# Kernel optimization log

Measured on AMD Instinct MI355X. Metric: run time of the kernel, lower is better.

Reference implementation:

```python
import jax, jax.numpy as jnp
import numpy as np

N_EMBD = 1024
N_HEAD = 16
LN_EPS = 1e-5

def setup_inputs() -> dict:
    key = jax.random.key(0)
    ks = jax.random.split(key, 12)
    B, T, C = 2, 2048, N_EMBD
    s = lambda k, shape, scale=0.02: (jax.random.normal(k, shape, dtype=jnp.float32) * scale)
    return {
        "x": jax.random.normal(ks[0], (B, T, C), dtype=jnp.float32),
        "ln1_g": jnp.ones((C,), jnp.float32),
        "ln1_b": jnp.zeros((C,), jnp.float32),
        "W_attn": s(ks[1], (C, 3 * C)),
        "b_attn": jnp.zeros((3 * C,), jnp.float32),
        "W_o": s(ks[2], (C, C)),
        "b_o": jnp.zeros((C,), jnp.float32),
        "ln2_g": jnp.ones((C,), jnp.float32),
        "ln2_b": jnp.zeros((C,), jnp.float32),
        "W_fc": s(ks[3], (C, 4 * C)),
        "b_fc": jnp.zeros((4 * C,), jnp.float32),
        "W_fc2": s(ks[4], (4 * C, C)),
        "b_fc2": jnp.zeros((C,), jnp.float32),
    }

def _layernorm(x, g, b):
    mu = jnp.mean(x, axis=-1, keepdims=True)
    var = jnp.mean(jnp.square(x - mu), axis=-1, keepdims=True)
    return (x - mu) * jax.lax.rsqrt(var + LN_EPS) * g + b

def reference(x, ln1_g, ln1_b, W_attn, b_attn, W_o, b_o, ln2_g, ln2_b, W_fc, b_fc, W_fc2, b_fc2):
    B, T, C = x.shape
    H, D = N_HEAD, C // N_HEAD
    # ---- attention branch (use_cache=False: T_total == T, causal mask) ----
    h = _layernorm(x, ln1_g, ln1_b)
    qkv = h @ W_attn + b_attn                       # [B,T,3C]
    q, k, v = jnp.split(qkv, 3, axis=-1)
    q = q.reshape(B, T, H, D).transpose(0, 2, 1, 3)  # [B,H,T,D]
    k = k.reshape(B, T, H, D).transpose(0, 2, 1, 3)
    v = v.reshape(B, T, H, D).transpose(0, 2, 1, 3)
    w = jnp.einsum('bhqd,bhkd->bhqk', q, k) / jnp.sqrt(jnp.float32(D))  # [B,H,T,T]
    causal = jnp.tril(jnp.ones((T, T), dtype=bool))
    w = jnp.where(causal, w, jnp.float32(-jnp.inf))
    w = jax.nn.softmax(w, axis=-1)
    y = jnp.einsum('bhqk,bhkd->bhqd', w, v)          # [B,H,T,D]
    y = y.transpose(0, 2, 1, 3).reshape(B, T, C)
    x = x + (y @ W_o + b_o)
    # ---- MLP branch ----
    h2 = _layernorm(x, ln2_g, ln2_b)
    h2 = jax.nn.gelu(h2 @ W_fc + b_fc, approximate=True)  # tanh approx, matches nn.GELU('tanh')
    x = x + (h2 @ W_fc2 + b_fc2)
    return x
```

## Files before the change

### kernel.cpp

```cpp
#include <hip/hip_runtime.h>


typedef unsigned short u16;
typedef unsigned int u32;
typedef __attribute__((ext_vector_type(8))) short v8s;
typedef __attribute__((ext_vector_type(4))) float v4f;

#define GAS __attribute__((address_space(1)))
#define LAS __attribute__((address_space(3)))

__device__ __forceinline__ u16 f2bf(float f) {
  u32 u = __float_as_uint(f);
  u = (u + 0x7FFF + ((u >> 16) & 1)) >> 16;
  return (u16)u;
}
__device__ __forceinline__ float bf2f(u16 h) {
  return __uint_as_float(((u32)h) << 16);
}
__device__ __forceinline__ float fast_tanh(float x) {
  return 1.f - 2.f / (1.f + __expf(2.f * x));
}

__global__ __launch_bounds__(256)
void wtrans(const float* __restrict__ W, u16* __restrict__ Wt, int K, int N) {
  __shared__ float tile[32][33];
  const int n0 = blockIdx.x << 5, k0 = blockIdx.y << 5;
  const int r = threadIdx.x >> 5, c = threadIdx.x & 31;
#pragma unroll
  for (int i = 0; i < 4; ++i)
    tile[r + 8 * i][c] = W[(size_t)(k0 + r + 8 * i) * N + n0 + c];
  __syncthreads();
#pragma unroll
  for (int i = 0; i < 4; ++i)
    Wt[(size_t)(n0 + r + 8 * i) * K + k0 + c] = f2bf(tile[c][r + 8 * i]);
}

__global__ __launch_bounds__(256)
void ln_bf16(const float* __restrict__ x, const float* __restrict__ g,
             const float* __restrict__ be, u16* __restrict__ out) {
  constexpr int C = 1024;
  const int row = blockIdx.x, t = threadIdx.x;
  const float4 v = ((const float4*)(x + (size_t)row * C))[t];
  float s = v.x + v.y + v.z + v.w;
#pragma unroll
  for (int m = 32; m >= 1; m >>= 1) s += __shfl_xor(s, m);
  __shared__ float red[4], red2[4];
  if ((t & 63) == 0) red[t >> 6] = s;
  __syncthreads();
  const float mu = (red[0] + red[1] + red[2] + red[3]) * (1.f / C);
  const float dx = v.x - mu, dy = v.y - mu, dz = v.z - mu, dw = v.w - mu;
  float s2 = dx * dx + dy * dy + dz * dz + dw * dw;
#pragma unroll
  for (int m = 32; m >= 1; m >>= 1) s2 += __shfl_xor(s2, m);
  if ((t & 63) == 0) red2[t >> 6] = s2;
  __syncthreads();
  const float var = (red2[0] + red2[1] + red2[2] + red2[3]) * (1.f / C);
  const float rs = rsqrtf(var + 1e-5f);
  const int c = t << 2;
  u16 o0 = f2bf(dx * rs * g[c + 0] + be[c + 0]);
  u16 o1 = f2bf(dy * rs * g[c + 1] + be[c + 1]);
  u16 o2 = f2bf(dz * rs * g[c + 2] + be[c + 2]);
  u16 o3 = f2bf(dw * rs * g[c + 3] + be[c + 3]);
  uint2 pk;
  pk.x = (u32)o0 | ((u32)o1 << 16);
  pk.y = (u32)o2 | ((u32)o3 << 16);
  *(uint2*)(out + (size_t)row * C + c) = pk;
}

template <int EPI>
__global__ __launch_bounds__(256)
void gemm_bt_p(const u16* __restrict__ A, const u16* __restrict__ Bt,
               const float* __restrict__ bias, const float* __restrict__ res,
               void* __restrict__ outp, int M, int N, int K) {
  __shared__ u16 As[4][128 * 32];
  __shared__ u16 Bs[4][128 * 32];
  const int tid = threadIdx.x;
  const int wave = tid >> 6, lane = tid & 63;
  const int m0 = blockIdx.y << 7, n0 = blockIdx.x << 7;

  v4f acc[4][4];
  const v4f vz = {0.f, 0.f, 0.f, 0.f};
#pragma unroll
  for (int i = 0; i < 4; ++i)
#pragma unroll
    for (int j = 0; j < 4; ++j) acc[i][j] = vz;

  const int wm = (wave >> 1) << 6, wn = (wave & 1) << 6;
  const int sr = lane >> 2;
  const int sc = (lane & 3) << 3;
  const int fr = lane & 15;
  const int fk = (lane >> 4) << 3;
  const int c0 = wave << 1;

  const u16* gA0 = A + (size_t)(m0 + c0 * 16 + sr) * K + sc;
  const u16* gA1 = A + (size_t)(m0 + c0 * 16 + 16 + sr) * K + sc;
  const u16* gB0 = Bt + (size_t)(n0 + c0 * 16 + sr) * K + sc;
  const u16* gB1 = Bt + (size_t)(n0 + c0 * 16 + 16 + sr) * K + sc;
  const int aoff = c0 * 512;

  const u32 asb = (u32)(size_t)(LAS const u16*)&As[0][0];
  const u32 bsb = (u32)(size_t)(LAS const u16*)&Bs[0][0];
  const u32 afrag = (u32)(((wm + fr) << 6) + (fk << 1));
  const u32 bfrag = (u32)(((wn + fr) << 6) + (fk << 1));

  const int nk = K >> 5;

#define P128_ISSUE(t, bf)                                                        \
  do {                                                                           \
    const int k0_ = (t) << 5;                                                    \
    __builtin_amdgcn_global_load_lds((GAS const u32*)(gA0 + k0_),                \
                                     (LAS u32*)(As[bf] + aoff), 16, 0, 0);       \
    __builtin_amdgcn_global_load_lds((GAS const u32*)(gA1 + k0_),                \
                                     (LAS u32*)(As[bf] + aoff + 512), 16, 0, 0); \
    __builtin_amdgcn_global_load_lds((GAS const u32*)(gB0 + k0_),                \
                                     (LAS u32*)(Bs[bf] + aoff), 16, 0, 0);       \
    __builtin_amdgcn_global_load_lds((GAS const u32*)(gB1 + k0_),                \
                                     (LAS u32*)(Bs[bf] + aoff + 512), 16, 0, 0); \
  } while (0)

  P128_ISSUE(0, 0);
  P128_ISSUE(1, 1);
  P128_ISSUE(2, 2);

  auto compute = [&](int kt) __attribute__((always_inline)) {
    const u32 ab = asb + ((u32)(kt & 3) << 13) + afrag;
    const u32 bb = bsb + ((u32)(kt & 3) << 13) + bfrag;
    v8s a0, a1, a2, a3, b0, b1, b2, b3;
    asm volatile("ds_read_b128 %0, %1 offset:0"    : "=v"(a0) : "v"(ab));
    asm volatile("ds_read_b128 %0, %1 offset:1024" : "=v"(a1) : "v"(ab));
    asm volatile("ds_read_b128 %0, %1 offset:2048" : "=v"(a2) : "v"(ab));
    asm volatile("ds_read_b128 %0, %1 offset:3072" : "=v"(a3) : "v"(ab));
    asm volatile("ds_read_b128 %0, %1 offset:0"    : "=v"(b0) : "v"(bb));
    asm volatile("ds_read_b128 %0, %1 offset:1024" : "=v"(b1) : "v"(bb));
    asm volatile("ds_read_b128 %0, %1 offset:2048" : "=v"(b2) : "v"(bb));
    asm volatile("ds_read_b128 %0, %1 offset:3072" : "=v"(b3) : "v"(bb));
    asm volatile("s_waitcnt lgkmcnt(0)"
                 : "+v"(a0), "+v"(a1), "+v"(a2), "+v"(a3),
                   "+v"(b0), "+v"(b1), "+v"(b2), "+v"(b3)
                 :
                 : "memory");
    acc[0][0] = __builtin_amdgcn_mfma_f32_16x16x32_bf16(a0, b0, acc[0][0], 0, 0, 0);
    acc[0][1] = __builtin_amdgcn_mfma_f32_16x16x32_bf16(a0, b1, acc[0][1], 0, 0, 0);
    acc[0][2] = __builtin_amdgcn_mfma_f32_16x16x32_bf16(a0, b2, acc[0][2], 0, 0, 0);
    acc[0][3] = __builtin_amdgcn_mfma_f32_16x16x32_bf16(a0, b3, acc[0][3], 0, 0, 0);
    acc[1][0] = __builtin_amdgcn_mfma_f32_16x16x32_bf16(a1, b0, acc[1][0], 0, 0, 0);
    acc[1][1] = __builtin_amdgcn_mfma_f32_16x16x32_bf16(a1, b1, acc[1][1], 0, 0, 0);
    acc[1][2] = __builtin_amdgcn_mfma_f32_16x16x32_bf16(a1, b2, acc[1][2], 0, 0, 0);
    acc[1][3] = __builtin_amdgcn_mfma_f32_16x16x32_bf16(a1, b3, acc[1][3], 0, 0, 0);
    acc[2][0] = __builtin_amdgcn_mfma_f32_16x16x32_bf16(a2, b0, acc[2][0], 0, 0, 0);
    acc[2][1] = __builtin_amdgcn_mfma_f32_16x16x32_bf16(a2, b1, acc[2][1], 0, 0, 0);
    acc[2][2] = __builtin_amdgcn_mfma_f32_16x16x32_bf16(a2, b2, acc[2][2], 0, 0, 0);
    acc[2][3] = __builtin_amdgcn_mfma_f32_16x16x32_bf16(a2, b3, acc[2][3], 0, 0, 0);
    acc[3][0] = __builtin_amdgcn_mfma_f32_16x16x32_bf16(a3, b0, acc[3][0], 0, 0, 0);
    acc[3][1] = __builtin_amdgcn_mfma_f32_16x16x32_bf16(a3, b1, acc[3][1], 0, 0, 0);
    acc[3][2] = __builtin_amdgcn_mfma_f32_16x16x32_bf16(a3, b2, acc[3][2], 0, 0, 0);
    acc[3][3] = __builtin_amdgcn_mfma_f32_16x16x32_bf16(a3, b3, acc[3][3], 0, 0, 0);
  };

  for (int kt = 0; kt < nk - 3; ++kt) {
    asm volatile("s_waitcnt vmcnt(8)" ::: "memory");
    __builtin_amdgcn_s_barrier();
    P128_ISSUE(kt + 3, (kt + 3) & 3);
    compute(kt);
  }
  asm volatile("s_waitcnt vmcnt(8)" ::: "memory");
  __builtin_amdgcn_s_barrier();
  compute(nk - 3);
  asm volatile("s_waitcnt vmcnt(4)" ::: "memory");
  __builtin_amdgcn_s_barrier();
  compute(nk - 2);
  asm volatile("s_waitcnt vmcnt(0)" ::: "memory");
  __builtin_amdgcn_s_barrier();
  compute(nk - 1);
#undef P128_ISSUE

  const int er = (lane >> 4) << 2;
#pragma unroll
  for (int mi = 0; mi < 4; ++mi) {
#pragma unroll
    for (int ni = 0; ni < 4; ++ni) {
      const int col = n0 + wn + ni * 16 + fr;
      const float bcol = bias[col];
#pragma unroll
      for (int r = 0; r < 4; ++r) {
        const int row = m0 + wm + mi * 16 + er + r;
        float v = acc[mi][ni][r] + bcol;
        if constexpr (EPI == 1) {
          const float t = fast_tanh(0.7978845608028654f * (v + 0.044715f * v * v * v));
          v = 0.5f * v * (1.f + t);
        }
        if constexpr (EPI == 2) {
          v += res[(size_t)row * N + col];
          ((float*)outp)[(size_t)row * N + col] = v;
        } else {
          ((u16*)outp)[(size_t)row * N + col] = f2bf(v);
        }
      }
    }
  }
}

template <int EPI>
__global__ __launch_bounds__(256)
void gemm_bt_p6(const u16* __restrict__ A, const u16* __restrict__ Bt,
                const float* __restrict__ bias, const float* __restrict__ res,
                void* __restrict__ outp, int M, int N, int K) {
  __shared__ u16 As[6][128 * 32];
  __shared__ u16 Bs[6][128 * 32];
  const int tid = threadIdx.x;
  const int wave = tid >> 6, lane = tid & 63;
  const int wg = blockIdx.y * (int)gridDim.x + blockIdx.x;
  const int xcd = wg & 7;
  const int seq = wg >> 3;
  const int bx = seq & 7;
  const int by = ((seq >> 3) << 3) + xcd;
  const int m0 = by << 7, n0 = bx << 7;

  v4f acc[4][4];
  const v4f vz = {0.f, 0.f, 0.f, 0.f};
#pragma unroll
  for (int i = 0; i < 4; ++i)
#pragma unroll
    for (int j = 0; j < 4; ++j) acc[i][j] = vz;

  const int wm = (wave >> 1) << 6, wn = (wave & 1) << 6;
  const int sr = lane >> 2;
  const int sc = (lane & 3) << 3;
  const int fr = lane & 15;
  const int fk = (lane >> 4) << 3;
  const int c0 = wave << 1;

  const u16* gA0 = A + (size_t)(m0 + c0 * 16 + sr) * K + sc;
  const u16* gA1 = A + (size_t)(m0 + c0 * 16 + 16 + sr) * K + sc;
  const u16* gB0 = Bt + (size_t)(n0 + c0 * 16 + sr) * K + sc;
  const u16* gB1 = Bt + (size_t)(n0 + c0 * 16 + 16 + sr) * K + sc;
  const int aoff = c0 * 512;

  const u32 asb = (u32)(size_t)(LAS const u16*)&As[0][0];
  const u32 bsb = (u32)(size_t)(LAS const u16*)&Bs[0][0];
  const u32 afrag = (u32)(((wm + fr) << 6) + (fk << 1));
  const u32 bfrag = (u32)(((wn + fr) << 6) + (fk << 1));

  const int nk = K >> 5;

#define P6_ISSUE(t, bf)                                                          \
  do {                                                                           \
    const int k0_ = (t) << 5;                                                    \
    __builtin_amdgcn_global_load_lds((GAS const u32*)(gA0 + k0_),                \
                                     (LAS u32*)(As[bf] + aoff), 16, 0, 0);       \
    __builtin_amdgcn_global_load_lds((GAS const u32*)(gA1 + k0_),                \
                                     (LAS u32*)(As[bf] + aoff + 512), 16, 0, 0); \
    __builtin_amdgcn_global_load_lds((GAS const u32*)(gB0 + k0_),                \
                                     (LAS u32*)(Bs[bf] + aoff), 16, 0, 0);       \
    __builtin_amdgcn_global_load_lds((GAS const u32*)(gB1 + k0_),                \
                                     (LAS u32*)(Bs[bf] + aoff + 512), 16, 0, 0); \
  } while (0)

  P6_ISSUE(0, 0);
  P6_ISSUE(1, 1);
  P6_ISSUE(2, 2);
  P6_ISSUE(3, 3);
  P6_ISSUE(4, 4);

  auto compute = [&](int cbuf) __attribute__((always_inline)) {
    const u32 ab = asb + ((u32)cbuf << 13) + afrag;
    const u32 bb = bsb + ((u32)cbuf << 13) + bfrag;
    v8s a0, a1, a2, a3, b0, b1, b2, b3;
    asm volatile("ds_read_b128 %0, %1 offset:0"    : "=v"(a0) : "v"(ab));
    asm volatile("ds_read_b128 %0, %1 offset:1024" : "=v"(a1) : "v"(ab));
    asm volatile("ds_read_b128 %0, %1 offset:2048" : "=v"(a2) : "v"(ab));
    asm volatile("ds_read_b128 %0, %1 offset:3072" : "=v"(a3) : "v"(ab));
    asm volatile("ds_read_b128 %0, %1 offset:0"    : "=v"(b0) : "v"(bb));
    asm volatile("ds_read_b128 %0, %1 offset:1024" : "=v"(b1) : "v"(bb));
    asm volatile("ds_read_b128 %0, %1 offset:2048" : "=v"(b2) : "v"(bb));
    asm volatile("ds_read_b128 %0, %1 offset:3072" : "=v"(b3) : "v"(bb));
    asm volatile("s_waitcnt lgkmcnt(0)"
                 : "+v"(a0), "+v"(a1), "+v"(a2), "+v"(a3),
                   "+v"(b0), "+v"(b1), "+v"(b2), "+v"(b3)
                 :
                 : "memory");
    acc[0][0] = __builtin_amdgcn_mfma_f32_16x16x32_bf16(a0, b0, acc[0][0], 0, 0, 0);
    acc[0][1] = __builtin_amdgcn_mfma_f32_16x16x32_bf16(a0, b1, acc[0][1], 0, 0, 0);
    acc[0][2] = __builtin_amdgcn_mfma_f32_16x16x32_bf16(a0, b2, acc[0][2], 0, 0, 0);
    acc[0][3] = __builtin_amdgcn_mfma_f32_16x16x32_bf16(a0, b3, acc[0][3], 0, 0, 0);
    acc[1][0] = __builtin_amdgcn_mfma_f32_16x16x32_bf16(a1, b0, acc[1][0], 0, 0, 0);
    acc[1][1] = __builtin_amdgcn_mfma_f32_16x16x32_bf16(a1, b1, acc[1][1], 0, 0, 0);
    acc[1][2] = __builtin_amdgcn_mfma_f32_16x16x32_bf16(a1, b2, acc[1][2], 0, 0, 0);
    acc[1][3] = __builtin_amdgcn_mfma_f32_16x16x32_bf16(a1, b3, acc[1][3], 0, 0, 0);
    acc[2][0] = __builtin_amdgcn_mfma_f32_16x16x32_bf16(a2, b0, acc[2][0], 0, 0, 0);
    acc[2][1] = __builtin_amdgcn_mfma_f32_16x16x32_bf16(a2, b1, acc[2][1], 0, 0, 0);
    acc[2][2] = __builtin_amdgcn_mfma_f32_16x16x32_bf16(a2, b2, acc[2][2], 0, 0, 0);
    acc[2][3] = __builtin_amdgcn_mfma_f32_16x16x32_bf16(a2, b3, acc[2][3], 0, 0, 0);
    acc[3][0] = __builtin_amdgcn_mfma_f32_16x16x32_bf16(a3, b0, acc[3][0], 0, 0, 0);
    acc[3][1] = __builtin_amdgcn_mfma_f32_16x16x32_bf16(a3, b1, acc[3][1], 0, 0, 0);
    acc[3][2] = __builtin_amdgcn_mfma_f32_16x16x32_bf16(a3, b2, acc[3][2], 0, 0, 0);
    acc[3][3] = __builtin_amdgcn_mfma_f32_16x16x32_bf16(a3, b3, acc[3][3], 0, 0, 0);
  };

  int cb = 0;
  int pb = 5;
  for (int kt = 0; kt < nk - 5; ++kt) {
    asm volatile("s_waitcnt vmcnt(16)" ::: "memory");
    __builtin_amdgcn_s_barrier();
    P6_ISSUE(kt + 5, pb);
    compute(cb);
    cb = (cb == 5) ? 0 : cb + 1;
    pb = (pb == 5) ? 0 : pb + 1;
  }
  asm volatile("s_waitcnt vmcnt(16)" ::: "memory");
  __builtin_amdgcn_s_barrier();
  compute(cb); cb = (cb == 5) ? 0 : cb + 1;
  asm volatile("s_waitcnt vmcnt(12)" ::: "memory");
  __builtin_amdgcn_s_barrier();
  compute(cb); cb = (cb == 5) ? 0 : cb + 1;
  asm volatile("s_waitcnt vmcnt(8)" ::: "memory");
  __builtin_amdgcn_s_barrier();
  compute(cb); cb = (cb == 5) ? 0 : cb + 1;
  asm volatile("s_waitcnt vmcnt(4)" ::: "memory");
  __builtin_amdgcn_s_barrier();
  compute(cb); cb = (cb == 5) ? 0 : cb + 1;
  asm volatile("s_waitcnt vmcnt(0)" ::: "memory");
  __builtin_amdgcn_s_barrier();
  compute(cb);
#undef P6_ISSUE

  const int er = (lane >> 4) << 2;
#pragma unroll
  for (int mi = 0; mi < 4; ++mi) {
#pragma unroll
    for (int ni = 0; ni < 4; ++ni) {
      const int col = n0 + wn + ni * 16 + fr;
      const float bcol = bias[col];
#pragma unroll
      for (int r = 0; r < 4; ++r) {
        const int row = m0 + wm + mi * 16 + er + r;
        float v = acc[mi][ni][r] + bcol;
        if constexpr (EPI == 1) {
          const float t = fast_tanh(0.7978845608028654f * (v + 0.044715f * v * v * v));
          v = 0.5f * v * (1.f + t);
        }
        if constexpr (EPI == 2) {
          v += res[(size_t)row * N + col];
          ((float*)outp)[(size_t)row * N + col] = v;
        } else {
          ((u16*)outp)[(size_t)row * N + col] = f2bf(v);
        }
      }
    }
  }
}

template <int EPI>
__global__ __launch_bounds__(256)
void gemm_bt_n64(const u16* __restrict__ A, const u16* __restrict__ Bt,
                 const float* __restrict__ bias, const float* __restrict__ res,
                 void* __restrict__ outp, int M, int N, int K) {
  __shared__ u16 As[4][128 * 32];
  __shared__ u16 Bs[4][64 * 32];
  const int tid = threadIdx.x;
  const int wave = tid >> 6, lane = tid & 63;
  const int m0 = blockIdx.y << 7, n0 = blockIdx.x << 6;

  v4f acc[4][2];
  const v4f vz = {0.f, 0.f, 0.f, 0.f};
#pragma unroll
  for (int i = 0; i < 4; ++i)
#pragma unroll
    for (int j = 0; j < 2; ++j) acc[i][j] = vz;

  const int wm = (wave >> 1) << 6, wn = (wave & 1) << 5;
  const int sr = lane >> 2;
  const int sc = (lane & 3) << 3;
  const int fr = lane & 15;
  const int fk = (lane >> 4) << 3;

  const u16* gA0 = A + (size_t)(m0 + wave * 32 + sr) * K + sc;
  const u16* gA1 = A + (size_t)(m0 + wave * 32 + 16 + sr) * K + sc;
  const u16* gB0 = Bt + (size_t)(n0 + wave * 16 + sr) * K + sc;
  const int aoff = wave * 1024;
  const int boff = wave * 512;

  const u32 asb = (u32)(size_t)(LAS const u16*)&As[0][0];
  const u32 bsb = (u32)(size_t)(LAS const u16*)&Bs[0][0];
  const u32 afrag = (u32)(((wm + fr) << 6) + (fk << 1));
  const u32 bfrag = (u32)(((wn + fr) << 6) + (fk << 1));

  const int nk = K >> 5;

#define N64_ISSUE(t, bf)                                                      \
  do {                                                                        \
    const int k0_ = (t) << 5;                                                 \
    __builtin_amdgcn_global_load_lds((GAS const u32*)(gA0 + k0_),             \
                                     (LAS u32*)(As[bf] + aoff), 16, 0, 0);    \
    __builtin_amdgcn_global_load_lds((GAS const u32*)(gA1 + k0_),             \
                                     (LAS u32*)(As[bf] + aoff + 512), 16, 0, 0); \
    __builtin_amdgcn_global_load_lds((GAS const u32*)(gB0 + k0_),             \
                                     (LAS u32*)(Bs[bf] + boff), 16, 0, 0);    \
  } while (0)

  N64_ISSUE(0, 0);
  N64_ISSUE(1, 1);
  N64_ISSUE(2, 2);

  auto compute = [&](int kt) __attribute__((always_inline)) {
    const u32 ab = asb + ((u32)(kt & 3) << 13) + afrag;
    const u32 bb = bsb + ((u32)(kt & 3) << 12) + bfrag;
    v8s a0, a1, a2, a3, b0, b1;
    asm volatile("ds_read_b128 %0, %1 offset:0"    : "=v"(a0) : "v"(ab));
    asm volatile("ds_read_b128 %0, %1 offset:1024" : "=v"(a1) : "v"(ab));
    asm volatile("ds_read_b128 %0, %1 offset:2048" : "=v"(a2) : "v"(ab));
    asm volatile("ds_read_b128 %0, %1 offset:3072" : "=v"(a3) : "v"(ab));
    asm volatile("ds_read_b128 %0, %1 offset:0"    : "=v"(b0) : "v"(bb));
    asm volatile("ds_read_b128 %0, %1 offset:1024" : "=v"(b1) : "v"(bb));
    asm volatile("s_waitcnt lgkmcnt(0)"
                 : "+v"(a0), "+v"(a1), "+v"(a2), "+v"(a3), "+v"(b0), "+v"(b1)
                 :
                 : "memory");
    acc[0][0] = __builtin_amdgcn_mfma_f32_16x16x32_bf16(a0, b0, acc[0][0], 0, 0, 0);
    acc[0][1] = __builtin_amdgcn_mfma_f32_16x16x32_bf16(a0, b1, acc[0][1], 0, 0, 0);
    acc[1][0] = __builtin_amdgcn_mfma_f32_16x16x32_bf16(a1, b0, acc[1][0], 0, 0, 0);
    acc[1][1] = __builtin_amdgcn_mfma_f32_16x16x32_bf16(a1, b1, acc[1][1], 0, 0, 0);
    acc[2][0] = __builtin_amdgcn_mfma_f32_16x16x32_bf16(a2, b0, acc[2][0], 0, 0, 0);
    acc[2][1] = __builtin_amdgcn_mfma_f32_16x16x32_bf16(a2, b1, acc[2][1], 0, 0, 0);
    acc[3][0] = __builtin_amdgcn_mfma_f32_16x16x32_bf16(a3, b0, acc[3][0], 0, 0, 0);
    acc[3][1] = __builtin_amdgcn_mfma_f32_16x16x32_bf16(a3, b1, acc[3][1], 0, 0, 0);
  };

  for (int kt = 0; kt < nk - 2; ++kt) {
    asm volatile("s_waitcnt vmcnt(6)" ::: "memory");
    __builtin_amdgcn_s_barrier();
    if (kt + 3 < nk) N64_ISSUE(kt + 3, (kt + 3) & 3);
    compute(kt);
  }
  asm volatile("s_waitcnt vmcnt(3)" ::: "memory");
  __builtin_amdgcn_s_barrier();
  compute(nk - 2);
  asm volatile("s_waitcnt vmcnt(0)" ::: "memory");
  __builtin_amdgcn_s_barrier();
  compute(nk - 1);
#undef N64_ISSUE

  const int er = (lane >> 4) << 2;
#pragma unroll
  for (int mi = 0; mi < 4; ++mi) {
#pragma unroll
    for (int ni = 0; ni < 2; ++ni) {
      const int col = n0 + wn + ni * 16 + fr;
      const float bcol = bias[col];
#pragma unroll
      for (int r = 0; r < 4; ++r) {
        const int row = m0 + wm + mi * 16 + er + r;
        float v = acc[mi][ni][r] + bcol;
        if constexpr (EPI == 1) {
          const float t = fast_tanh(0.7978845608028654f * (v + 0.044715f * v * v * v));
          v = 0.5f * v * (1.f + t);
        }
        if constexpr (EPI == 2) {
          v += res[(size_t)row * N + col];
          ((float*)outp)[(size_t)row * N + col] = v;
        } else {
          ((u16*)outp)[(size_t)row * N + col] = f2bf(v);
        }
      }
    }
  }
}

__global__ __launch_bounds__(256)
void transpose_v(const u16* __restrict__ qkv, u16* __restrict__ Vt) {
  __shared__ u16 tile[64][65];
  const int t0 = blockIdx.x << 6;
  const int bh = blockIdx.y;
  const int b = bh >> 4, h = bh & 15;
  const int r4 = threadIdx.x >> 6, c = threadIdx.x & 63;
#pragma unroll
  for (int i = 0; i < 16; ++i) {
    const int r = r4 * 16 + i;
    tile[r][c] = qkv[(size_t)(b * 2048 + t0 + r) * 3072 + 2048 + h * 64 + c];
  }
  __syncthreads();
#pragma unroll
  for (int i = 0; i < 16; ++i) {
    const int d = r4 * 16 + i;
    Vt[(size_t)bh * 64 * 2048 + (size_t)d * 2048 + t0 + c] = tile[c][d];
  }
}

constexpr int PSTR = 88;

template <bool MASKED>
__device__ __forceinline__ void attn_sub(
    const v8s (&kf)[4][2], const v8s (&vfr)[4][2], const v8s (&qf)[2],
    v4f (&ot)[4], float& m_i, float& l_i, u16* __restrict__ pw,
    const int kb, const int qrow, const int fr, const int fg) {
  const v4f vz = {0.f, 0.f, 0.f, 0.f};
  v4f st[4];
#pragma unroll
  for (int ks = 0; ks < 4; ++ks) {
    st[ks] = vz;
    st[ks] = __builtin_amdgcn_mfma_f32_16x16x32_bf16(kf[ks][0], qf[0], st[ks], 0, 0, 0);
    st[ks] = __builtin_amdgcn_mfma_f32_16x16x32_bf16(kf[ks][1], qf[1], st[ks], 0, 0, 0);
  }
  const int q = qrow + fr;
  float e[4][4];
  float mt = -1e30f;
#pragma unroll
  for (int ks = 0; ks < 4; ++ks)
#pragma unroll
    for (int r = 0; r < 4; ++r) {
      float v = st[ks][r] * 0.125f;
      if (MASKED) v = (kb + ks * 16 + fg * 4 + r <= q) ? v : -1e30f;
      e[ks][r] = v;
      mt = fmaxf(mt, v);
    }
  mt = fmaxf(mt, __shfl_xor(mt, 16));
  mt = fmaxf(mt, __shfl_xor(mt, 32));
  const float m_new = fmaxf(m_i, mt);
  const float alpha = __expf(m_i - m_new);
  m_i = m_new;
  float ls = 0.f;
#pragma unroll
  for (int ks = 0; ks < 4; ++ks)
#pragma unroll
    for (int r = 0; r < 4; ++r) {
      e[ks][r] = __expf(e[ks][r] - m_new);
      ls += e[ks][r];
    }
  ls += __shfl_xor(ls, 16);
  ls += __shfl_xor(ls, 32);
  l_i = l_i * alpha + ls;
#pragma unroll
  for (int ds = 0; ds < 4; ++ds) ot[ds] *= alpha;
#pragma unroll
  for (int ks = 0; ks < 4; ++ks) {
    ushort4 pk4;
    pk4.x = f2bf(e[ks][0]);
    pk4.y = f2bf(e[ks][1]);
    pk4.z = f2bf(e[ks][2]);
    pk4.w = f2bf(e[ks][3]);
    *(ushort4*)&pw[fr * PSTR + ks * 16 + fg * 4] = pk4;
  }
  const v8s pf0 = *(const v8s*)&pw[fr * PSTR + fg * 8];
  const v8s pf1 = *(const v8s*)&pw[fr * PSTR + 32 + fg * 8];
#pragma unroll
  for (int ds = 0; ds < 4; ++ds) {
    ot[ds] = __builtin_amdgcn_mfma_f32_16x16x32_bf16(vfr[ds][0], pf0, ot[ds], 0, 0, 0);
    ot[ds] = __builtin_amdgcn_mfma_f32_16x16x32_bf16(vfr[ds][1], pf1, ot[ds], 0, 0, 0);
  }
}

__global__ __launch_bounds__(256)
void attn_kernel(const u16* __restrict__ qkv, const u16* __restrict__ Vt,
                 u16* __restrict__ y) {
  constexpr int T = 2048, D = 64, C = 1024, QS = 3072;
  __shared__ alignas(16) u16 Ktile[2][64 * 64];
  __shared__ alignas(16) u16 Vtile[2][64 * 64];
  __shared__ alignas(16) u16 Pw[4][16 * PSTR];

  const int tid = threadIdx.x, wave = tid >> 6, lane = tid & 63;
  const int fr = lane & 15, fg = lane >> 4;
  const int bh = blockIdx.y, b = bh >> 4, h = bh & 15;
  const int ta = blockIdx.x, tb = 31 - ta;
  const u16* qkvb = qkv + (size_t)b * T * QS + h * 64;
  const u16* Kg = qkvb + 1024;
  const u16* Vh = Vt + (size_t)bh * D * T;
  u16* pw = &Pw[wave][0];

  const int rowA = ta * 64 + wave * 16;
  const int rowB = tb * 64 + wave * 16;

  v8s qfA[2], qfB[2];
#pragma unroll
  for (int dh = 0; dh < 2; ++dh) {
    qfA[dh] = *(const v8s*)&qkvb[(size_t)(rowA + fr) * QS + dh * 32 + fg * 8];
    qfB[dh] = *(const v8s*)&qkvb[(size_t)(rowB + fr) * QS + dh * 32 + fg * 8];
  }

  const v4f vz = {0.f, 0.f, 0.f, 0.f};
  v4f otA[4], otB[4];
#pragma unroll
  for (int ds = 0; ds < 4; ++ds) { otA[ds] = vz; otB[ds] = vz; }
  float mA = -1e30f, lA = 0.f, mB = -1e30f, lB = 0.f;

  const int srow = lane >> 3;
  const int sg0 = lane & 7;

  const int nt = tb + 1;
  {
#pragma unroll
    for (int cc = 0; cc < 2; ++cc) {
      const int r0 = wave * 16 + cc * 8;
      const int rr = r0 + srow;
      const int gg = sg0 ^ (rr & 7);
      __builtin_amdgcn_global_load_lds(
          (GAS const u32*)(Kg + (size_t)rr * QS + gg * 8),
          (LAS u32*)(Ktile[0] + r0 * 64), 16, 0, 0);
      __builtin_amdgcn_global_load_lds(
          (GAS const u32*)(Vh + (size_t)rr * T + gg * 8),
          (LAS u32*)(Vtile[0] + r0 * 64), 16, 0, 0);
    }
  }
  for (int kt = 0; kt < nt; ++kt) {
    __syncthreads();
    if (kt + 1 < nt) {
      const int kb1 = (kt + 1) << 6;
      const int nb = (kt + 1) & 1;
#pragma unroll
      for (int cc = 0; cc < 2; ++cc) {
        const int r0 = wave * 16 + cc * 8;
        const int rr = r0 + srow;
        const int gg = sg0 ^ (rr & 7);
        __builtin_amdgcn_global_load_lds(
            (GAS const u32*)(Kg + (size_t)(kb1 + rr) * QS + gg * 8),
            (LAS u32*)(Ktile[nb] + r0 * 64), 16, 0, 0);
        __builtin_amdgcn_global_load_lds(
            (GAS const u32*)(Vh + (size_t)rr * T + kb1 + gg * 8),
            (LAS u32*)(Vtile[nb] + r0 * 64), 16, 0, 0);
      }
    }
    const u16* Kt = Ktile[kt & 1];
    const u16* Vi = Vtile[kt & 1];
    const int kb = kt << 6;
    const int swz = fr & 7;
    v8s kf[4][2], vfr[4][2];
#pragma unroll
    for (int ks = 0; ks < 4; ++ks) {
      const int rr = ks * 16 + fr;
      kf[ks][0] = *(const v8s*)&Kt[rr * 64 + ((0 + fg) ^ swz) * 8];
      kf[ks][1] = *(const v8s*)&Kt[rr * 64 + ((4 + fg) ^ swz) * 8];
      vfr[ks][0] = *(const v8s*)&Vi[rr * 64 + ((0 + fg) ^ swz) * 8];
      vfr[ks][1] = *(const v8s*)&Vi[rr * 64 + ((4 + fg) ^ swz) * 8];
    }
    if (kt < ta) {
      attn_sub<false>(kf, vfr, qfA, otA, mA, lA, pw, kb, rowA, fr, fg);
      attn_sub<false>(kf, vfr, qfB, otB, mB, lB, pw, kb, rowB, fr, fg);
    } else if (kt == ta) {
      attn_sub<true>(kf, vfr, qfA, otA, mA, lA, pw, kb, rowA, fr, fg);
      attn_sub<false>(kf, vfr, qfB, otB, mB, lB, pw, kb, rowB, fr, fg);
    } else if (kt < tb) {
      attn_sub<false>(kf, vfr, qfB, otB, mB, lB, pw, kb, rowB, fr, fg);
    } else {
      attn_sub<true>(kf, vfr, qfB, otB, mB, lB, pw, kb, rowB, fr, fg);
    }
  }

  const float invA = 1.f / lA, invB = 1.f / lB;
#pragma unroll
  for (int ds = 0; ds < 4; ++ds) {
    ushort4 a4, b4;
    a4.x = f2bf(otA[ds][0] * invA);
    a4.y = f2bf(otA[ds][1] * invA);
    a4.z = f2bf(otA[ds][2] * invA);
    a4.w = f2bf(otA[ds][3] * invA);
    b4.x = f2bf(otB[ds][0] * invB);
    b4.y = f2bf(otB[ds][1] * invB);
    b4.z = f2bf(otB[ds][2] * invB);
    b4.w = f2bf(otB[ds][3] * invB);
    *(ushort4*)&y[(size_t)(b * T + rowA + fr) * C + h * D + ds * 16 + fg * 4] = a4;
    *(ushort4*)&y[(size_t)(b * T + rowB + fr) * C + h * D + ds * 16 + fg * 4] = b4;
  }
}

extern "C" void kernel_launch(void* const* d_in, const int* in_sizes, int n_in,
                              void* d_out, int out_size, void* d_ws, size_t ws_size,
                              hipStream_t stream) {
  const float* x      = (const float*)d_in[0];
  const float* ln1_g  = (const float*)d_in[1];
  const float* ln1_b  = (const float*)d_in[2];
  const float* W_attn = (const float*)d_in[3];
  const float* b_attn = (const float*)d_in[4];
  const float* W_o    = (const float*)d_in[5];
  const float* b_o    = (const float*)d_in[6];
  const float* ln2_g  = (const float*)d_in[7];
  const float* ln2_b  = (const float*)d_in[8];
  const float* W_fc   = (const float*)d_in[9];
  const float* b_fc   = (const float*)d_in[10];
  const float* W_fc2  = (const float*)d_in[11];
  const float* b_fc2  = (const float*)d_in[12];
  float* out = (float*)d_out;
  char* ws = (char*)d_ws;

  const size_t MB = 1u << 20;
  u16* Wattn_t = (u16*)(ws + 0 * MB);
  u16* Wo_t    = (u16*)(ws + 6 * MB);
  u16* Wfc_t   = (u16*)(ws + 8 * MB);
  u16* Wfc2_t  = (u16*)(ws + 16 * MB);
  float* x1    = (float*)(ws + 24 * MB);
  u16* h1      = (u16*)(ws + 40 * MB);
  u16* qkv     = (u16*)(ws + 48 * MB);
  u16* Vt      = (u16*)(ws + 88 * MB);
  u16* yb      = (u16*)(ws + 40 * MB);
  u16* h2      = (u16*)(ws + 48 * MB);
  u16* ab      = (u16*)(ws + 56 * MB);

  wtrans<<<dim3(3072 / 32, 1024 / 32), 256, 0, stream>>>(W_attn, Wattn_t, 1024, 3072);
  wtrans<<<dim3(1024 / 32, 1024 / 32), 256, 0, stream>>>(W_o, Wo_t, 1024, 1024);
  wtrans<<<dim3(4096 / 32, 1024 / 32), 256, 0, stream>>>(W_fc, Wfc_t, 1024, 4096);
  wtrans<<<dim3(1024 / 32, 4096 / 32), 256, 0, stream>>>(W_fc2, Wfc2_t, 4096, 1024);

  ln_bf16<<<4096, 256, 0, stream>>>(x, ln1_g, ln1_b, h1);
  gemm_bt_p<0><<<dim3(3072 / 128, 4096 / 128), 256, 0, stream>>>(
      h1, Wattn_t, b_attn, nullptr, qkv, 4096, 3072, 1024);
  transpose_v<<<dim3(2048 / 64, 32), 256, 0, stream>>>(qkv, Vt);
  attn_kernel<<<dim3(16, 32), 256, 0, stream>>>(qkv, Vt, yb);
  gemm_bt_n64<2><<<dim3(1024 / 64, 4096 / 128), 256, 0, stream>>>(
      yb, Wo_t, b_o, x, x1, 4096, 1024, 1024);
  ln_bf16<<<4096, 256, 0, stream>>>(x1, ln2_g, ln2_b, h2);
  gemm_bt_p<1><<<dim3(4096 / 128, 4096 / 128), 256, 0, stream>>>(
      h2, Wfc_t, b_fc, nullptr, ab, 4096, 4096, 1024);
  gemm_bt_p6<2><<<dim3(1024 / 128, 4096 / 128), 256, 0, stream>>>(
      ab, Wfc2_t, b_fc2, x1, out, 4096, 1024, 4096);
}
```

Before: 363.0 us.

## Double-buffer LDS fragments in GEMM and fold p6 kernel into templated gemm_bt_p

The 128x128 GEMM mainloop now reads the next k-step's LDS fragments into a second register set while the MFMAs for the current step run. A sched_barrier keeps the ordering fixed so LDS read latency hides behind matrix math. The separate 6-stage gemm_bt_p6 kernel is removed, and the FC2 GEMM now uses the 4-stage kernel with an XCD-aware block remap template flag. This costs extra VGPRs for the second fragment set, and FC2 loses its deeper global prefetch.

```diff
diff --git a/kernel.cpp b/kernel.cpp
--- a/kernel.cpp
+++ b/kernel.cpp
@@ -67,7 +67,7 @@
   *(uint2*)(out + (size_t)row * C + c) = pk;
 }
 
-template <int EPI>
+template <int EPI, int REMAP>
 __global__ __launch_bounds__(256)
 void gemm_bt_p(const u16* __restrict__ A, const u16* __restrict__ Bt,
                const float* __restrict__ bias, const float* __restrict__ res,
@@ -76,7 +76,18 @@
   __shared__ u16 Bs[4][128 * 32];
   const int tid = threadIdx.x;
   const int wave = tid >> 6, lane = tid & 63;
-  const int m0 = blockIdx.y << 7, n0 = blockIdx.x << 7;
+  int bx, by;
+  if constexpr (REMAP) {
+    const int wg = blockIdx.y * (int)gridDim.x + blockIdx.x;
+    const int xcd = wg & 7;
+    const int seq = wg >> 3;
+    bx = seq & 7;
+    by = ((seq >> 3) << 3) + xcd;
+  } else {
+    bx = blockIdx.x;
+    by = blockIdx.y;
+  }
+  const int m0 = by << 7, n0 = bx << 7;
 
   v4f acc[4][4];
   const v4f vz = {0.f, 0.f, 0.f, 0.f};
@@ -118,211 +129,66 @@
                                      (LAS u32*)(Bs[bf] + aoff + 512), 16, 0, 0); \
   } while (0)
 
+  auto ldfr = [&](int kt, v8s (&a)[4], v8s (&b)[4]) __attribute__((always_inline)) {
+    const u32 ab = asb + ((u32)(kt & 3) << 13) + afrag;
+    const u32 bb = bsb + ((u32)(kt & 3) << 13) + bfrag;
+    asm volatile("ds_read_b128 %0, %1 offset:0"    : "=v"(a[0]) : "v"(ab));
+    asm volatile("ds_read_b128 %0, %1 offset:1024" : "=v"(a[1]) : "v"(ab));
+    asm volatile("ds_read_b128 %0, %1 offset:2048" : "=v"(a[2]) : "v"(ab));
+    asm volatile("ds_read_b128 %0, %1 offset:3072" : "=v"(a[3]) : "v"(ab));
+    asm volatile("ds_read_b128 %0, %1 offset:0"    : "=v"(b[0]) : "v"(bb));
+    asm volatile("ds_read_b128 %0, %1 offset:1024" : "=v"(b[1]) : "v"(bb));
+    asm volatile("ds_read_b128 %0, %1 offset:2048" : "=v"(b[2]) : "v"(bb));
+    asm volatile("ds_read_b128 %0, %1 offset:3072" : "=v"(b[3]) : "v"(bb));
+  };
+  auto wait8 = [&](v8s (&a)[4], v8s (&b)[4]) __attribute__((always_inline)) {
+    asm volatile("s_waitcnt lgkmcnt(0)"
+                 : "+v"(a[0]), "+v"(a[1]), "+v"(a[2]), "+v"(a[3]),
+                   "+v"(b[0]), "+v"(b[1]), "+v"(b[2]), "+v"(b[3])
+                 :
+                 : "memory");
+  };
+  auto mfma16 = [&](v8s (&a)[4], v8s (&b)[4]) __attribute__((always_inline)) {
+#pragma unroll
+    for (int i = 0; i < 4; ++i)
+#pragma unroll
+      for (int j = 0; j < 4; ++j)
+        acc[i][j] = __builtin_amdgcn_mfma_f32_16x16x32_bf16(a[i], b[j], acc[i][j], 0, 0, 0);
+  };
+
+  v8s aX[4], bX[4], aY[4], bY[4];
+
   P128_ISSUE(0, 0);
   P128_ISSUE(1, 1);
   P128_ISSUE(2, 2);
-
-  auto compute = [&](int kt) __attribute__((always_inline)) {
-    const u32 ab = asb + ((u32)(kt & 3) << 13) + afrag;
-    const u32 bb = bsb + ((u32)(kt & 3) << 13) + bfrag;
-    v8s a0, a1, a2, a3, b0, b1, b2, b3;
-    asm volatile("ds_read_b128 %0, %1 offset:0"    : "=v"(a0) : "v"(ab));
-    asm volatile("ds_read_b128 %0, %1 offset:1024" : "=v"(a1) : "v"(ab));
-    asm volatile("ds_read_b128 %0, %1 offset:2048" : "=v"(a2) : "v"(ab));
-    asm volatile("ds_read_b128 %0, %1 offset:3072" : "=v"(a3) : "v"(ab));
-    asm volatile("ds_read_b128 %0, %1 offset:0"    : "=v"(b0) : "v"(bb));
-    asm volatile("ds_read_b128 %0, %1 offset:1024" : "=v"(b1) : "v"(bb));
-    asm volatile("ds_read_b128 %0, %1 offset:2048" : "=v"(b2) : "v"(bb));
-    asm volatile("ds_read_b128 %0, %1 offset:3072" : "=v"(b3) : "v"(bb));
-    asm volatile("s_waitcnt lgkmcnt(0)"
-                 : "+v"(a0), "+v"(a1), "+v"(a2), "+v"(a3),
-                   "+v"(b0), "+v"(b1), "+v"(b2), "+v"(b3)
-                 :
-                 : "memory");
-    acc[0][0] = __builtin_amdgcn_mfma_f32_16x16x32_bf16(a0, b0, acc[0][0], 0, 0, 0);
-    acc[0][1] = __builtin_amdgcn_mfma_f32_16x16x32_bf16(a0, b1, acc[0][1], 0, 0, 0);
-    acc[0][2] = __builtin_amdgcn_mfma_f32_16x16x32_bf16(a0, b2, acc[0][2], 0, 0, 0);
-    acc[0][3] = __builtin_amdgcn_mfma_f32_16x16x32_bf16(a0, b3, acc[0][3], 0, 0, 0);
-    acc[1][0] = __builtin_amdgcn_mfma_f32_16x16x32_bf16(a1, b0, acc[1][0], 0, 0, 0);
-    acc[1][1] = __builtin_amdgcn_mfma_f32_16x16x32_bf16(a1, b1, acc[1][1], 0, 0, 0);
-    acc[1][2] = __builtin_amdgcn_mfma_f32_16x16x32_bf16(a1, b2, acc[1][2], 0, 0, 0);
-    acc[1][3] = __builtin_amdgcn_mfma_f32_16x16x32_bf16(a1, b3, acc[1][3], 0, 0, 0);
-    acc[2][0] = __builtin_amdgcn_mfma_f32_16x16x32_bf16(a2, b0, acc[2][0], 0, 0, 0);
-    acc[2][1] = __builtin_amdgcn_mfma_f32_16x16x32_bf16(a2, b1, acc[2][1], 0, 0, 0);
-    acc[2][2] = __builtin_amdgcn_mfma_f32_16x16x32_bf16(a2, b2, acc[2][2], 0, 0, 0);
-    acc[2][3] = __builtin_amdgcn_mfma_f32_16x16x32_bf16(a2, b3, acc[2][3], 0, 0, 0);
-    acc[3][0] = __builtin_amdgcn_mfma_f32_16x16x32_bf16(a3, b0, acc[3][0], 0, 0, 0);
-    acc[3][1] = __builtin_amdgcn_mfma_f32_16x16x32_bf16(a3, b1, acc[3][1], 0, 0, 0);
-    acc[3][2] = __builtin_amdgcn_mfma_f32_16x16x32_bf16(a3, b2, acc[3][2], 0, 0, 0);
-    acc[3][3] = __builtin_amdgcn_mfma_f32_16x16x32_bf16(a3, b3, acc[3][3], 0, 0, 0);
-  };
-
-  for (int kt = 0; kt < nk - 3; ++kt) {
-    asm volatile("s_waitcnt vmcnt(8)" ::: "memory");
-    __builtin_amdgcn_s_barrier();
-    P128_ISSUE(kt + 3, (kt + 3) & 3);
-    compute(kt);
-  }
   asm volatile("s_waitcnt vmcnt(8)" ::: "memory");
   __builtin_amdgcn_s_barrier();
-  compute(nk - 3);
-  asm volatile("s_waitcnt vmcnt(4)" ::: "memory");
-  __builtin_amdgcn_s_barrier();
-  compute(nk - 2);
+  ldfr(0, aX, bX);
+  wait8(aX, bX);
+
+  auto step4 = [&](int k, v8s (&ca)[4], v8s (&cb)[4],
+                   v8s (&na)[4], v8s (&nb)[4]) __attribute__((always_inline)) {
+    asm volatile("s_waitcnt vmcnt(4)" ::: "memory");
+    __builtin_amdgcn_s_barrier();
+    ldfr(k + 1, na, nb);
+    if (k + 3 < nk) P128_ISSUE(k + 3, (k + 3) & 3);
+    __builtin_amdgcn_sched_barrier(0);
+    mfma16(ca, cb);
+    wait8(na, nb);
+  };
+
+  for (int kt = 0; kt < nk - 2; kt += 2) {
+    step4(kt, aX, bX, aY, bY);
+    step4(kt + 1, aY, bY, aX, bX);
+  }
   asm volatile("s_waitcnt vmcnt(0)" ::: "memory");
   __builtin_amdgcn_s_barrier();
-  compute(nk - 1);
+  ldfr(nk - 1, aY, bY);
+  __builtin_amdgcn_sched_barrier(0);
+  mfma16(aX, bX);
+  wait8(aY, bY);
+  mfma16(aY, bY);
 #undef P128_ISSUE
-
-  const int er = (lane >> 4) << 2;
-#pragma unroll
-  for (int mi = 0; mi < 4; ++mi) {
-#pragma unroll
-    for (int ni = 0; ni < 4; ++ni) {
-      const int col = n0 + wn + ni * 16 + fr;
-      const float bcol = bias[col];
-#pragma unroll
-      for (int r = 0; r < 4; ++r) {
-        const int row = m0 + wm + mi * 16 + er + r;
-        float v = acc[mi][ni][r] + bcol;
-        if constexpr (EPI == 1) {
-          const float t = fast_tanh(0.7978845608028654f * (v + 0.044715f * v * v * v));
-          v = 0.5f * v * (1.f + t);
-        }
-        if constexpr (EPI == 2) {
-          v += res[(size_t)row * N + col];
-          ((float*)outp)[(size_t)row * N + col] = v;
-        } else {
-          ((u16*)outp)[(size_t)row * N + col] = f2bf(v);
-        }
-      }
-    }
-  }
-}
-
-template <int EPI>
-__global__ __launch_bounds__(256)
-void gemm_bt_p6(const u16* __restrict__ A, const u16* __restrict__ Bt,
-                const float* __restrict__ bias, const float* __restrict__ res,
-                void* __restrict__ outp, int M, int N, int K) {
-  __shared__ u16 As[6][128 * 32];
-  __shared__ u16 Bs[6][128 * 32];
-  const int tid = threadIdx.x;
-  const int wave = tid >> 6, lane = tid & 63;
-  const int wg = blockIdx.y * (int)gridDim.x + blockIdx.x;
-  const int xcd = wg & 7;
-  const int seq = wg >> 3;
-  const int bx = seq & 7;
-  const int by = ((seq >> 3) << 3) + xcd;
-  const int m0 = by << 7, n0 = bx << 7;
-
-  v4f acc[4][4];
-  const v4f vz = {0.f, 0.f, 0.f, 0.f};
-#pragma unroll
-  for (int i = 0; i < 4; ++i)
-#pragma unroll
-    for (int j = 0; j < 4; ++j) acc[i][j] = vz;
-
-  const int wm = (wave >> 1) << 6, wn = (wave & 1) << 6;
-  const int sr = lane >> 2;
-  const int sc = (lane & 3) << 3;
-  const int fr = lane & 15;
-  const int fk = (lane >> 4) << 3;
-  const int c0 = wave << 1;
-
-  const u16* gA0 = A + (size_t)(m0 + c0 * 16 + sr) * K + sc;
-  const u16* gA1 = A + (size_t)(m0 + c0 * 16 + 16 + sr) * K + sc;
-  const u16* gB0 = Bt + (size_t)(n0 + c0 * 16 + sr) * K + sc;
-  const u16* gB1 = Bt + (size_t)(n0 + c0 * 16 + 16 + sr) * K + sc;
-  const int aoff = c0 * 512;
-
-  const u32 asb = (u32)(size_t)(LAS const u16*)&As[0][0];
-  const u32 bsb = (u32)(size_t)(LAS const u16*)&Bs[0][0];
-  const u32 afrag = (u32)(((wm + fr) << 6) + (fk << 1));
-  const u32 bfrag = (u32)(((wn + fr) << 6) + (fk << 1));
-
-  const int nk = K >> 5;
-
-#define P6_ISSUE(t, bf)                                                          \
-  do {                                                                           \
-    const int k0_ = (t) << 5;                                                    \
-    __builtin_amdgcn_global_load_lds((GAS const u32*)(gA0 + k0_),                \
-                                     (LAS u32*)(As[bf] + aoff), 16, 0, 0);       \
-    __builtin_amdgcn_global_load_lds((GAS const u32*)(gA1 + k0_),                \
-                                     (LAS u32*)(As[bf] + aoff + 512), 16, 0, 0); \
-    __builtin_amdgcn_global_load_lds((GAS const u32*)(gB0 + k0_),                \
-                                     (LAS u32*)(Bs[bf] + aoff), 16, 0, 0);       \
-    __builtin_amdgcn_global_load_lds((GAS const u32*)(gB1 + k0_),                \
-                                     (LAS u32*)(Bs[bf] + aoff + 512), 16, 0, 0); \
-  } while (0)
-
-  P6_ISSUE(0, 0);
-  P6_ISSUE(1, 1);
-  P6_ISSUE(2, 2);
-  P6_ISSUE(3, 3);
-  P6_ISSUE(4, 4);
-
-  auto compute = [&](int cbuf) __attribute__((always_inline)) {
-    const u32 ab = asb + ((u32)cbuf << 13) + afrag;
-    const u32 bb = bsb + ((u32)cbuf << 13) + bfrag;
-    v8s a0, a1, a2, a3, b0, b1, b2, b3;
-    asm volatile("ds_read_b128 %0, %1 offset:0"    : "=v"(a0) : "v"(ab));
-    asm volatile("ds_read_b128 %0, %1 offset:1024" : "=v"(a1) : "v"(ab));
-    asm volatile("ds_read_b128 %0, %1 offset:2048" : "=v"(a2) : "v"(ab));
-    asm volatile("ds_read_b128 %0, %1 offset:3072" : "=v"(a3) : "v"(ab));
-    asm volatile("ds_read_b128 %0, %1 offset:0"    : "=v"(b0) : "v"(bb));
-    asm volatile("ds_read_b128 %0, %1 offset:1024" : "=v"(b1) : "v"(bb));
-    asm volatile("ds_read_b128 %0, %1 offset:2048" : "=v"(b2) : "v"(bb));
-    asm volatile("ds_read_b128 %0, %1 offset:3072" : "=v"(b3) : "v"(bb));
-    asm volatile("s_waitcnt lgkmcnt(0)"
-                 : "+v"(a0), "+v"(a1), "+v"(a2), "+v"(a3),
-                   "+v"(b0), "+v"(b1), "+v"(b2), "+v"(b3)
-                 :
-                 : "memory");
-    acc[0][0] = __builtin_amdgcn_mfma_f32_16x16x32_bf16(a0, b0, acc[0][0], 0, 0, 0);
-    acc[0][1] = __builtin_amdgcn_mfma_f32_16x16x32_bf16(a0, b1, acc[0][1], 0, 0, 0);
-    acc[0][2] = __builtin_amdgcn_mfma_f32_16x16x32_bf16(a0, b2, acc[0][2], 0, 0, 0);
-    acc[0][3] = __builtin_amdgcn_mfma_f32_16x16x32_bf16(a0, b3, acc[0][3], 0, 0, 0);
-    acc[1][0] = __builtin_amdgcn_mfma_f32_16x16x32_bf16(a1, b0, acc[1][0], 0, 0, 0);
-    acc[1][1] = __builtin_amdgcn_mfma_f32_16x16x32_bf16(a1, b1, acc[1][1], 0, 0, 0);
-    acc[1][2] = __builtin_amdgcn_mfma_f32_16x16x32_bf16(a1, b2, acc[1][2], 0, 0, 0);
-    acc[1][3] = __builtin_amdgcn_mfma_f32_16x16x32_bf16(a1, b3, acc[1][3], 0, 0, 0);
-    acc[2][0] = __builtin_amdgcn_mfma_f32_16x16x32_bf16(a2, b0, acc[2][0], 0, 0, 0);
-    acc[2][1] = __builtin_amdgcn_mfma_f32_16x16x32_bf16(a2, b1, acc[2][1], 0, 0, 0);
-    acc[2][2] = __builtin_amdgcn_mfma_f32_16x16x32_bf16(a2, b2, acc[2][2], 0, 0, 0);
-    acc[2][3] = __builtin_amdgcn_mfma_f32_16x16x32_bf16(a2, b3, acc[2][3], 0, 0, 0);
-    acc[3][0] = __builtin_amdgcn_mfma_f32_16x16x32_bf16(a3, b0, acc[3][0], 0, 0, 0);
-    acc[3][1] = __builtin_amdgcn_mfma_f32_16x16x32_bf16(a3, b1, acc[3][1], 0, 0, 0);
-    acc[3][2] = __builtin_amdgcn_mfma_f32_16x16x32_bf16(a3, b2, acc[3][2], 0, 0, 0);
-    acc[3][3] = __builtin_amdgcn_mfma_f32_16x16x32_bf16(a3, b3, acc[3][3], 0, 0, 0);
-  };
-
-  int cb = 0;
-  int pb = 5;
-  for (int kt = 0; kt < nk - 5; ++kt) {
-    asm volatile("s_waitcnt vmcnt(16)" ::: "memory");
-    __builtin_amdgcn_s_barrier();
-    P6_ISSUE(kt + 5, pb);
-    compute(cb);
-    cb = (cb == 5) ? 0 : cb + 1;
-    pb = (pb == 5) ? 0 : pb + 1;
-  }
-  asm volatile("s_waitcnt vmcnt(16)" ::: "memory");
-  __builtin_amdgcn_s_barrier();
-  compute(cb); cb = (cb == 5) ? 0 : cb + 1;
-  asm volatile("s_waitcnt vmcnt(12)" ::: "memory");
-  __builtin_amdgcn_s_barrier();
-  compute(cb); cb = (cb == 5) ? 0 : cb + 1;
-  asm volatile("s_waitcnt vmcnt(8)" ::: "memory");
-  __builtin_amdgcn_s_barrier();
-  compute(cb); cb = (cb == 5) ? 0 : cb + 1;
-  asm volatile("s_waitcnt vmcnt(4)" ::: "memory");
-  __builtin_amdgcn_s_barrier();
-  compute(cb); cb = (cb == 5) ? 0 : cb + 1;
-  asm volatile("s_waitcnt vmcnt(0)" ::: "memory");
-  __builtin_amdgcn_s_barrier();
-  compute(cb);
-#undef P6_ISSUE
 
   const int er = (lane >> 4) << 2;
 #pragma unroll
@@ -699,15 +565,15 @@
   wtrans<<<dim3(1024 / 32, 4096 / 32), 256, 0, stream>>>(W_fc2, Wfc2_t, 4096, 1024);
 
   ln_bf16<<<4096, 256, 0, stream>>>(x, ln1_g, ln1_b, h1);
-  gemm_bt_p<0><<<dim3(3072 / 128, 4096 / 128), 256, 0, stream>>>(
+  gemm_bt_p<0, 0><<<dim3(3072 / 128, 4096 / 128), 256, 0, stream>>>(
       h1, Wattn_t, b_attn, nullptr, qkv, 4096, 3072, 1024);
   transpose_v<<<dim3(2048 / 64, 32), 256, 0, stream>>>(qkv, Vt);
   attn_kernel<<<dim3(16, 32), 256, 0, stream>>>(qkv, Vt, yb);
   gemm_bt_n64<2><<<dim3(1024 / 64, 4096 / 128), 256, 0, stream>>>(
       yb, Wo_t, b_o, x, x1, 4096, 1024, 1024);
   ln_bf16<<<4096, 256, 0, stream>>>(x1, ln2_g, ln2_b, h2);
-  gemm_bt_p<1><<<dim3(4096 / 128, 4096 / 128), 256, 0, stream>>>(
+  gemm_bt_p<1, 0><<<dim3(4096 / 128, 4096 / 128), 256, 0, stream>>>(
       h2, Wfc_t, b_fc, nullptr, ab, 4096, 4096, 1024);
-  gemm_bt_p6<2><<<dim3(1024 / 128, 4096 / 128), 256, 0, stream>>>(
+  gemm_bt_p<2, 1><<<dim3(1024 / 128, 4096 / 128), 256, 0, stream>>>(
       ab, Wfc2_t, b_fc2, x1, out, 4096, 1024, 4096);
 }
```

Measured after the change: 353.5 us. 1.03x faster.
